# Performance work log

Hardware: AMD Instinct MI355X
Metric: run time of the kernel (lower is better)

The kernel has to match this reference:

```python
import jax, jax.numpy as jnp
import numpy as np

B, S, D, H, DFF = 4, 1024, 1024, 16, 4096
DK = D // H
EPS = 1e-5

def _ln(x, g, b):
    m = jnp.mean(x, -1, keepdims=True)
    v = jnp.mean((x - m) ** 2, -1, keepdims=True)
    return (x - m) * jax.lax.rsqrt(v + EPS) * g + b

def setup_inputs() -> dict:
    key = jax.random.key(0)
    ks = jax.random.split(key, 24)
    std = 0.02
    def w(k, shp):
        return jax.random.normal(k, shp, jnp.float32) * std
    return {
        'x': jax.random.normal(ks[0], (B, S, D), jnp.float32),
        'wq': w(ks[1], (D, D)), 'bq': jnp.zeros((D,), jnp.float32),
        'wk': w(ks[2], (D, D)), 'bk': jnp.zeros((D,), jnp.float32),
        'wv': w(ks[3], (D, D)), 'bv': jnp.zeros((D,), jnp.float32),
        'wo': w(ks[4], (D, D)), 'bo': jnp.zeros((D,), jnp.float32),
        'rel_table': jax.random.normal(ks[5], (2 * 64 - 1, H), jnp.float32),
        'g1': jnp.ones((D,), jnp.float32), 'be1': jnp.zeros((D,), jnp.float32),
        'g2': jnp.ones((D,), jnp.float32), 'be2': jnp.zeros((D,), jnp.float32),
        'w1': w(ks[6], (D, DFF)), 'b1': jnp.zeros((DFF,), jnp.float32),
        'w2': w(ks[7], (DFF, D)), 'b2': jnp.zeros((D,), jnp.float32),
        'w3': w(ks[8], (D, D)), 'b3': jnp.zeros((D,), jnp.float32),
        'gf': jnp.ones((D,), jnp.float32), 'bf': jnp.zeros((D,), jnp.float32),
    }

def reference(x, wq, bq, wk, bk, wv, bv, wo, bo, rel_table,
              g1, be1, g2, be2, w1, b1, w2, b2, w3, b3, gf, bf):
    # --- pre-norm attention ---
    nx = _ln(x, g1, be1)
    def heads(w, b):
        return (nx @ w + b).reshape(B, S, H, DK).transpose(0, 2, 1, 3)  # [B,H,S,DK]
    Q, K, V = heads(wq, bq), heads(wk, bk), heads(wv, bv)
    scores = jnp.einsum('bhsd,bhtd->bhst', Q, K) / jnp.sqrt(jnp.float32(DK))
    # relative position bias, clamped to table range
    rel = jnp.arange(S)[None, :] - jnp.arange(S)[:, None] + 63
    rel = jnp.clip(rel, 0, 2 * 64 - 2)               # [S,S]
    bias = rel_table[rel].transpose(2, 0, 1)          # [H,S,S]
    scores = scores + bias[None]
    attn = jax.nn.softmax(scores, axis=-1)
    ctx = jnp.einsum('bhst,bhtd->bhsd', attn, V)
    ctx = ctx.transpose(0, 2, 1, 3).reshape(B, S, D)
    x = x + (ctx @ wo + bo)
    # --- feed-forward (with its own inner residuals) ---
    nx2 = _ln(x, g2, be2)
    ff1 = jax.nn.gelu(nx2 @ w1 + b1, approximate=False) @ w2 + b2
    y = nx2 + ff1
    ff2 = _ln(y, gf, bf) @ w3 + b3
    ff_out = y + ff2
    return x + ff_out
```

## Files before the change

### kernel.cpp

```cpp
#include <hip/hip_runtime.h>
#include <hip/hip_bf16.h>
#include <math.h>


constexpr int Bc = 4, Sc_ = 1024, Dc = 1024, Hc = 16, DKc = 64, DFFc = 4096;
constexpr int ROWS = Bc * Sc_;
constexpr int BK = 32;

typedef short short8 __attribute__((ext_vector_type(8)));
typedef __bf16 bf16x8 __attribute__((ext_vector_type(8)));
typedef float float4v __attribute__((ext_vector_type(4)));
typedef uint uint2v __attribute__((ext_vector_type(2)));

__device__ __forceinline__ float bf2f(ushort u) {
    union { uint i; float f; } v; v.i = ((uint)u) << 16; return v.f;
}
__device__ __forceinline__ ushort f2bf(float f) {
    union { float f; uint i; } v; v.f = f;
    uint r = v.i + 0x7FFF + ((v.i >> 16) & 1);
    return (ushort)(r >> 16);
}
__device__ __forceinline__ bf16x8 as_bf(short8 s) {
    union { short8 s; bf16x8 b; } u; u.s = s; return u.b;
}
__device__ __forceinline__ uint cvt_pk_bf16(float lo, float hi) {
    uint r;
    asm("v_cvt_pk_bf16_f32 %0, %1, %2" : "=v"(r) : "v"(lo), "v"(hi));
    return r;
}
__device__ __forceinline__ float exp2_hw(float x) {
    float r;
    asm("v_exp_f32 %0, %1" : "=v"(r) : "v"(x));
    return r;
}
__device__ __forceinline__ void async_copy16(void* lds, const void* g) {
    __builtin_amdgcn_global_load_lds((const __attribute__((address_space(1))) uint*)g,
                                     (__attribute__((address_space(3))) uint*)lds, 16, 0, 0);
}
__device__ __forceinline__ float gelu_f(float v) {
    float z = v * 0.70710678118654752f;
    float az = fabsf(z);
    float t = 1.f / (1.f + 0.3275911f * az);
    float p = ((((1.061405429f * t - 1.453152027f) * t) + 1.421413741f) * t
               - 0.284496736f) * t + 0.254829592f;
    float y = 1.f - p * t * __expf(-az * az);
    float er = (z < 0.f) ? -y : y;
    return 0.5f * v * (1.f + er);
}

__global__ void sentinel_kernel(float* __restrict__ out, int n) {
    int i = blockIdx.x * 256 + threadIdx.x;
    if (i < n) out[i] = 100.0f;
}

__global__ void bias3_kernel(const float* __restrict__ a, const float* __restrict__ b,
                             const float* __restrict__ c, float* __restrict__ o) {
    int i = blockIdx.x * 256 + threadIdx.x;
    if (i < 1024) o[i] = a[i];
    else if (i < 2048) o[i] = b[i - 1024];
    else if (i < 3072) o[i] = c[i - 2048];
}

__global__ __launch_bounds__(256) void wconv_kernel(const float* __restrict__ W,
                                                    ushort* __restrict__ Wt,
                                                    int K, int N) {
    __shared__ float T[64][65];
    const int kt = blockIdx.y * 64, nt = blockIdx.x * 64;
    const int tid = threadIdx.x;
#pragma unroll
    for (int it = 0; it < 4; it++) {
        int r = it * 16 + (tid >> 4), c = (tid & 15) * 4;
        float4v v = *reinterpret_cast<const float4v*>(W + (size_t)(kt + r) * N + nt + c);
        T[r][c] = v[0]; T[r][c + 1] = v[1]; T[r][c + 2] = v[2]; T[r][c + 3] = v[3];
    }
    __syncthreads();
    int n = tid >> 2, kc = (tid & 3) * 16;
    short8 a, b;
#pragma unroll
    for (int q = 0; q < 8; q++) {
        a[q] = (short)f2bf(T[kc + q][n]);
        b[q] = (short)f2bf(T[kc + 8 + q][n]);
    }
    ushort* dst = Wt + (size_t)(nt + n) * K + kt + kc;
    *reinterpret_cast<short8*>(dst) = a;
    *reinterpret_cast<short8*>(dst + 8) = b;
}

__global__ __launch_bounds__(256) void vconv_kernel(const ushort* __restrict__ V,
                                                    ushort* __restrict__ Vt) {
    __shared__ ushort T[64][65];
    const int bh = blockIdx.y;
    const int s0 = blockIdx.x * 64;
    const int tid = threadIdx.x;
    const int r = tid >> 2, c = (tid & 3) * 16;
    const ushort* src = V + ((size_t)bh * Sc_ + s0 + r) * DKc + c;
    short8 a = *reinterpret_cast<const short8*>(src);
    short8 b = *reinterpret_cast<const short8*>(src + 8);
#pragma unroll
    for (int q = 0; q < 8; q++) { T[r][c + q] = (ushort)a[q]; T[r][c + 8 + q] = (ushort)b[q]; }
    __syncthreads();
    const int dk = tid >> 2, sc2 = (tid & 3) * 16;
    short8 o0, o1;
#pragma unroll
    for (int q = 0; q < 8; q++) { o0[q] = (short)T[sc2 + q][dk]; o1[q] = (short)T[sc2 + 8 + q][dk]; }
    ushort* dst = Vt + ((size_t)bh * DKc + dk) * Sc_ + s0 + sc2;
    *reinterpret_cast<short8*>(dst) = o0;
    *reinterpret_cast<short8*>(dst + 8) = o1;
}

template<bool IN_F32>
__global__ __launch_bounds__(256) void ln_kernel(const void* __restrict__ xin,
                                                 const float* __restrict__ g,
                                                 const float* __restrict__ be,
                                                 ushort* __restrict__ out) {
    int row = blockIdx.x;
    int tid = threadIdx.x;
    float v0[4], s = 0.f, ss = 0.f;
#pragma unroll
    for (int i = 0; i < 4; i++) {
        int c = tid + i * 256;
        float f = IN_F32 ? ((const float*)xin)[(size_t)row * Dc + c]
                         : bf2f(((const ushort*)xin)[(size_t)row * Dc + c]);
        v0[i] = f; s += f; ss += f * f;
    }
#pragma unroll
    for (int off = 32; off > 0; off >>= 1) {
        s += __shfl_down(s, off);
        ss += __shfl_down(ss, off);
    }
    __shared__ float red[8];
    __shared__ float stat[2];
    int wave = tid >> 6, lane = tid & 63;
    if (lane == 0) { red[wave] = s; red[wave + 4] = ss; }
    __syncthreads();
    if (tid == 0) {
        float a = 0.f, b = 0.f;
        for (int w = 0; w < 4; w++) { a += red[w]; b += red[w + 4]; }
        stat[0] = a; stat[1] = b;
    }
    __syncthreads();
    float mean = stat[0] * (1.f / Dc);
    float var  = stat[1] * (1.f / Dc) - mean * mean;
    float inv  = rsqrtf(var + 1e-5f);
#pragma unroll
    for (int i = 0; i < 4; i++) {
        int c = tid + i * 256;
        float nv = (v0[i] - mean) * inv * g[c] + be[c];
        out[(size_t)row * Dc + c] = f2bf(nv);
    }
}

template<int BM, int BN, typename OutT>
__global__ __launch_bounds__(256) void gemm_bt(
    const ushort* __restrict__ Ag, const ushort* __restrict__ Wt,
    const float* __restrict__ biasg,
    const float* __restrict__ res1f,
    const ushort* __restrict__ resi1, const ushort* __restrict__ resi2,
    OutT* __restrict__ outg,
    int M, int N, int K, int do_gelu, int mode) {
    constexpr int WN = BN / 64;
    constexpr int WM = 4 / WN;
    constexpr int MI = BM / (WM * 16);
    constexpr int TSZ = (BM + BN) * BK;
    constexpr int TOT = (BM + BN) * 4;
    constexpr int LPT = TOT / 256;
    constexpr unsigned VM_L = 0x0F70 | (unsigned)LPT;
    __shared__ ushort Tile[3 * TSZ];
    const int tid = threadIdx.x;
    const int wave = tid >> 6, lane = tid & 63;
    const int quad = lane >> 4, l16 = lane & 15;
    const int m0 = blockIdx.x * BM, n0 = blockIdx.y * BN;
    const int wm = (wave / WN) * (MI * 16), wn = (wave % WN) * 64;

    float4v acc[MI][4];
    const float4v zero = {0.f, 0.f, 0.f, 0.f};
#pragma unroll
    for (int i = 0; i < MI; i++)
#pragma unroll
        for (int j = 0; j < 4; j++) acc[i][j] = zero;

    auto stage = [&](int buf, int k0) {
#pragma unroll
        for (int it = 0; it < LPT; it++) {
            int c = tid + it * 256;
            int row = c >> 2, kc = (c & 3) * 8;
            const ushort* src = (row < BM)
                ? Ag + (size_t)(m0 + row) * K + k0 + kc
                : Wt + (size_t)(n0 + row - BM) * K + k0 + kc;
            async_copy16(&Tile[buf * TSZ + c * 8], src);
        }
    };

    const int nit = K / BK;
    stage(0, 0);
    stage(1, BK);
    int bc = 0, bs = 2;
    for (int i = 0; i < nit; i++) {
        __builtin_amdgcn_sched_barrier(0);
        if (i + 1 < nit) __builtin_amdgcn_s_waitcnt(VM_L);
        else             __builtin_amdgcn_s_waitcnt(0x0F70);
        __builtin_amdgcn_s_barrier();
        __builtin_amdgcn_sched_barrier(0);
        if (i + 2 < nit) stage(bs, (i + 2) * BK);
        const ushort* Asb = &Tile[bc * TSZ];
        const ushort* Bsb = &Tile[bc * TSZ + BM * BK];
        short8 af[MI], bfr[4];
#pragma unroll
        for (int ii = 0; ii < MI; ii++)
            af[ii] = *reinterpret_cast<const short8*>(&Asb[(wm + ii * 16 + l16) * BK + quad * 8]);
#pragma unroll
        for (int j = 0; j < 4; j++)
            bfr[j] = *reinterpret_cast<const short8*>(&Bsb[(wn + j * 16 + l16) * BK + quad * 8]);
#pragma unroll
        for (int j = 0; j < 4; j++)
#pragma unroll
            for (int ii = 0; ii < MI; ii++)
                acc[ii][j] = __builtin_amdgcn_mfma_f32_16x16x32_bf16(as_bf(af[ii]), as_bf(bfr[j]), acc[ii][j], 0, 0, 0);
        bc = (bc == 2) ? 0 : bc + 1;
        bs = (bs == 2) ? 0 : bs + 1;
    }
    __builtin_amdgcn_s_barrier();

#pragma unroll
    for (int j = 0; j < 4; j++) {
        int cg = n0 + wn + j * 16 + l16;
        float bv = biasg ? biasg[cg] : 0.f;
#pragma unroll
        for (int i = 0; i < MI; i++) {
#pragma unroll
            for (int r = 0; r < 4; r++) {
                int rg = m0 + wm + i * 16 + quad * 4 + r;
                float v = acc[i][j][r] + bv;
                if (do_gelu) v = gelu_f(v);
                size_t idx = (size_t)rg * N + cg;
                if (res1f) v += res1f[idx];
                if (resi1) v += bf2f(resi1[idx]);
                if (resi2) v += bf2f(resi2[idx]);
                size_t dst;
                if (mode == 1) {
                    int which = cg >> 10, wr2 = cg & 1023;
                    int h = wr2 >> 6, dk = wr2 & 63;
                    int b = rg >> 10, s = rg & 1023;
                    dst = (size_t)which * ((size_t)ROWS * Dc)
                        + (((size_t)b * Hc + h) * Sc_ + s) * DKc + dk;
                } else dst = idx;
                if constexpr (sizeof(OutT) == 4) outg[dst] = v;
                else                             outg[dst] = f2bf(v);
            }
        }
    }
}

template<typename OutT>
__global__ __launch_bounds__(512, 2) void gemm8_bt(
    const ushort* __restrict__ Ag, const ushort* __restrict__ Wt,
    const float* __restrict__ biasg, OutT* __restrict__ outg,
    int N, int K, int do_gelu, int mode) {
    __shared__ ushort Al[2][16384];
    __shared__ ushort Bl[2][16384];
    const int tid = threadIdx.x;
    const int wave = tid >> 6, lane = tid & 63;
    const int quad = lane >> 4, l16 = lane & 15;
    const int wm = (wave >> 2) * 128, wn = (wave & 3) * 64;
    const int m0 = blockIdx.y * 256, n0 = blockIdx.x * 256;

    float4v acc[8][4];
    const float4v zero = {0.f, 0.f, 0.f, 0.f};
#pragma unroll
    for (int i = 0; i < 8; i++)
#pragma unroll
        for (int j = 0; j < 4; j++) acc[i][j] = zero;

    auto stageH = [&](int buf, int k0, int which) {
#pragma unroll
        for (int it = 0; it < 2; it++) {
            int s = tid + it * 512;
            int rl = s >> 3, pch = s & 7;
            int ch = pch ^ (rl & 7);
            const ushort* src; ushort* dst;
            if (which == 0)      { int row = ((rl >> 6) << 7) + (rl & 63);
                                   src = Ag + (size_t)(m0 + row) * K + k0 + ch * 8;
                                   dst = &Al[buf][s * 8]; }
            else if (which == 1) { int row = ((rl >> 5) << 6) + (rl & 31);
                                   src = Wt + (size_t)(n0 + row) * K + k0 + ch * 8;
                                   dst = &Bl[buf][s * 8]; }
            else if (which == 2) { int row = ((rl >> 5) << 6) + 32 + (rl & 31);
                                   src = Wt + (size_t)(n0 + row) * K + k0 + ch * 8;
                                   dst = &Bl[buf][8192 + s * 8]; }
            else                 { int row = ((rl >> 6) << 7) + 64 + (rl & 63);
                                   src = Ag + (size_t)(m0 + row) * K + k0 + ch * 8;
                                   dst = &Al[buf][8192 + s * 8]; }
            async_copy16(dst, src);
        }
    };

    const int rlA = ((wm >> 7) << 6) + l16;
    const int rlB = ((wn >> 6) << 5) + l16;
    const int sw  = l16 & 7;

    const int nt = K >> 6;
    stageH(0, 0, 0); stageH(0, 0, 1); stageH(0, 0, 2); stageH(0, 0, 3);

#define G8_SYNC(WHICH, VMLAST)                                            \
    __builtin_amdgcn_sched_barrier(0);                                    \
    if (more) { stageH(nbuf, knext, WHICH);                               \
                __builtin_amdgcn_sched_barrier(0);                        \
                __builtin_amdgcn_s_waitcnt(0x0F76);         \
    } else   { __builtin_amdgcn_s_waitcnt(VMLAST); }                      \
    __builtin_amdgcn_s_barrier();                                         \
    __builtin_amdgcn_sched_barrier(0);

#define G8_COMPUTE(QM, QN, LOADA)                                         \
    if (LOADA) {                                                          \
        _Pragma("unroll") for (int kk = 0; kk < 2; kk++)                  \
        _Pragma("unroll") for (int i = 0; i < 4; i++)                     \
            af[kk][i] = *reinterpret_cast<const short8*>(                 \
                &Al[buf][(QM) * 8192 + (rlA + i * 16) * 64 +              \
                         (((kk << 2) | quad) ^ sw) * 8]);                 \
    }                                                                     \
    _Pragma("unroll") for (int kk = 0; kk < 2; kk++)                      \
    _Pragma("unroll") for (int j = 0; j < 2; j++)                         \
        bfr[kk][j] = *reinterpret_cast<const short8*>(                    \
            &Bl[buf][(QN) * 8192 + (rlB + j * 16) * 64 +                  \
                     (((kk << 2) | quad) ^ sw) * 8]);                     \
    __builtin_amdgcn_s_setprio(1);                                        \
    _Pragma("unroll") for (int kk = 0; kk < 2; kk++)                      \
    _Pragma("unroll") for (int i = 0; i < 4; i++)                         \
    _Pragma("unroll") for (int j = 0; j < 2; j++)                         \
        acc[(QM) * 4 + i][(QN) * 2 + j] =                                 \
            __builtin_amdgcn_mfma_f32_16x16x32_bf16(                      \
                as_bf(af[kk][i]), as_bf(bfr[kk][j]),                      \
                acc[(QM) * 4 + i][(QN) * 2 + j], 0, 0, 0);                \
    __builtin_amdgcn_s_setprio(0);

    for (int t = 0; t < nt; ++t) {
        const int buf = t & 1, nbuf = buf ^ 1;
        const int knext = (t + 1) << 6;
        const bool more = (t + 1 < nt);
        short8 af[2][4], bfr[2][2];
        G8_SYNC(0, 0x0F74)  G8_COMPUTE(0, 0, true)
        G8_SYNC(1, 0x0F72)  G8_COMPUTE(0, 1, false)
        G8_SYNC(2, 0x0F70)  G8_COMPUTE(1, 0, true)
        G8_SYNC(3, 0x0F70)  G8_COMPUTE(1, 1, false)
    }
#undef G8_SYNC
#undef G8_COMPUTE

#pragma unroll
    for (int jg = 0; jg < 4; jg++) {
        int cg = n0 + wn + jg * 16 + l16;
        float bv = biasg ? biasg[cg] : 0.f;
#pragma unroll
        for (int ig = 0; ig < 8; ig++) {
#pragma unroll
            for (int r = 0; r < 4; r++) {
                int rg = m0 + wm + ig * 16 + quad * 4 + r;
                float v = acc[ig][jg][r] + bv;
                if (do_gelu) v = gelu_f(v);
                size_t dst;
                if (mode == 1) {
                    int which = cg >> 10, wr2 = cg & 1023;
                    int h = wr2 >> 6, dk = wr2 & 63;
                    int b = rg >> 10, s = rg & 1023;
                    dst = (size_t)which * ((size_t)ROWS * Dc)
                        + (((size_t)b * Hc + h) * Sc_ + s) * DKc + dk;
                } else dst = (size_t)rg * N + cg;
                if constexpr (sizeof(OutT) == 4) outg[dst] = v;
                else                             outg[dst] = f2bf(v);
            }
        }
    }
}

__global__ __launch_bounds__(256, 4) void attn_kernel(
    const ushort* __restrict__ Qg, const ushort* __restrict__ Kg,
    const ushort* __restrict__ Vt, const float* __restrict__ relg,
    ushort* __restrict__ ctxg) {
    __shared__ ushort Kl[2][2048];
    __shared__ ushort Vl[2][2048];
    __shared__ float Tpad[1088];
    constexpr float L2E = 1.44269504f;

    const int blk = blockIdx.x;
    const int vb = (blk & 7) * 128 + (blk >> 3);
    const int bh = vb >> 4;
    const int qblk = vb & 15;
    const int h = bh & (Hc - 1);
    const int b = bh >> 4;
    const int qb = qblk * 64;
    const int tid = threadIdx.x;
    const int wave = tid >> 6, lane = tid & 63;
    const int quad = lane >> 4, l16 = lane & 15;
    const int ql = wave * 16 + l16;

    const ushort* Kbh  = Kg + (size_t)bh * Sc_ * DKc;
    const ushort* Vtbh = Vt + (size_t)bh * DKc * Sc_;

    auto stage = [&](int buf, int t0) {
        {
            int r = tid >> 3, ch = tid & 7;
            const ushort* src = Kbh + (size_t)(t0 + r) * DKc + ((ch ^ (r & 7)) * 8);
            async_copy16(&Kl[buf][tid * 8], src);
        }
        {
            int d = tid >> 2, ch = tid & 3;
            const ushort* src = Vtbh + (size_t)d * Sc_ + t0 + ((ch ^ ((d >> 1) & 3)) * 8);
            async_copy16(&Vl[buf][tid * 8], src);
        }
    };

    stage(0, 0);

    for (int j = tid; j < 1087; j += 256) {
        int r = min(max(j - qb, 0), 126);
        Tpad[j] = relg[r * Hc + h];
    }

    short8 aQ[2];
    {
        const ushort* qrow = Qg + ((size_t)bh * Sc_ + qb + ql) * DKc + quad * 8;
#pragma unroll
        for (int f = 0; f < 2; f++) {
            short8 v = *reinterpret_cast<const short8*>(qrow + f * 32);
#pragma unroll
            for (int e = 0; e < 8; e++) v[e] = (short)f2bf(bf2f((ushort)v[e]) * 0.125f);
            aQ[f] = v;
        }
    }
    __syncthreads();

    float4v accO[4];
#pragma unroll
    for (int i = 0; i < 4; i++) accO[i] = float4v{0.f, 0.f, 0.f, 0.f};
    float m = -1e30f, lsum = 0.f;
    float ml2 = m * L2E;
    const int srcA = ((quad & 1) * 2) * 16 + l16;
    const int srcB = srcA + 16;
    const bool hi = quad >= 2;

    auto compute = [&](int buf, int t0) {
        short8 vf[4];
#pragma unroll
        for (int dt = 0; dt < 4; dt++) {
            int d = dt * 16 + l16;
            vf[dt] = *reinterpret_cast<const short8*>(
                &Vl[buf][d * 32 + ((quad ^ ((l16 >> 1) & 3)) * 8)]);
        }
        short8 kf[2][2];
#pragma unroll
        for (int kt = 0; kt < 2; kt++)
#pragma unroll
            for (int f = 0; f < 2; f++)
                kf[kt][f] = *reinterpret_cast<const short8*>(
                    &Kl[buf][(kt * 16 + l16) * 64 + (((f * 4 + quad) ^ (l16 & 7)) * 8)]);

        const int jb = t0 + quad * 4 - ql + 63;
        float4v c0 = { Tpad[jb],      Tpad[jb + 1],  Tpad[jb + 2],  Tpad[jb + 3]  };
        float4v c1 = { Tpad[jb + 16], Tpad[jb + 17], Tpad[jb + 18], Tpad[jb + 19] };

        float4v s0 = __builtin_amdgcn_mfma_f32_16x16x32_bf16(as_bf(kf[0][0]), as_bf(aQ[0]), c0, 0, 0, 0);
        s0 = __builtin_amdgcn_mfma_f32_16x16x32_bf16(as_bf(kf[0][1]), as_bf(aQ[1]), s0, 0, 0, 0);
        float4v s1 = __builtin_amdgcn_mfma_f32_16x16x32_bf16(as_bf(kf[1][0]), as_bf(aQ[0]), c1, 0, 0, 0);
        s1 = __builtin_amdgcn_mfma_f32_16x16x32_bf16(as_bf(kf[1][1]), as_bf(aQ[1]), s1, 0, 0, 0);

        float lt = fmaxf(fmaxf(fmaxf(s0[0], s0[1]), fmaxf(s0[2], s0[3])),
                         fmaxf(fmaxf(s1[0], s1[1]), fmaxf(s1[2], s1[3])));
        if (!__all(lt <= m + 8.f)) {
            float tmax = fmaxf(lt, __shfl_xor(lt, 16));
            tmax = fmaxf(tmax, __shfl_xor(tmax, 32));
            float mn = fmaxf(m, tmax);
            float sc = exp2_hw((m - mn) * L2E);
            m = mn; ml2 = m * L2E;
            lsum *= sc;
#pragma unroll
            for (int dt = 0; dt < 4; dt++)
#pragma unroll
                for (int r = 0; r < 4; r++) accO[dt][r] *= sc;
        }
        float p0[4], p1[4];
#pragma unroll
        for (int r = 0; r < 4; r++) {
            p0[r] = exp2_hw(fmaf(s0[r], L2E, -ml2));
            p1[r] = exp2_hw(fmaf(s1[r], L2E, -ml2));
        }
        lsum += ((p0[0] + p0[1]) + (p0[2] + p0[3]))
              + ((p1[0] + p1[1]) + (p1[2] + p1[3]));

        uint w0 = cvt_pk_bf16(p0[0], p0[1]);
        uint w1 = cvt_pk_bf16(p0[2], p0[3]);
        uint w2 = cvt_pk_bf16(p1[0], p1[1]);
        uint w3 = cvt_pk_bf16(p1[2], p1[3]);
        uint a0 = __shfl(w0, srcA), a1 = __shfl(w1, srcA);
        uint a2 = __shfl(w2, srcA), a3 = __shfl(w3, srcA);
        uint b0 = __shfl(w0, srcB), b1 = __shfl(w1, srcB);
        uint b2 = __shfl(w2, srcB), b3 = __shfl(w3, srcB);
        union { uint u[4]; short8 s; } pf;
        pf.u[0] = hi ? a2 : a0;
        pf.u[1] = hi ? a3 : a1;
        pf.u[2] = hi ? b2 : b0;
        pf.u[3] = hi ? b3 : b1;

#pragma unroll
        for (int dt = 0; dt < 4; dt++)
            accO[dt] = __builtin_amdgcn_mfma_f32_16x16x32_bf16(as_bf(vf[dt]), as_bf(pf.s), accO[dt], 0, 0, 0);
    };

    for (int t0 = 0; t0 < Sc_; t0 += 64) {
        __builtin_amdgcn_sched_barrier(0);
        __builtin_amdgcn_s_waitcnt(0x0F70);
        __builtin_amdgcn_s_barrier();
        __builtin_amdgcn_sched_barrier(0);
        stage(1, t0 + 32);
        __builtin_amdgcn_sched_barrier(0);
        compute(0, t0);

        __builtin_amdgcn_sched_barrier(0);
        __builtin_amdgcn_s_waitcnt(0x0F70);
        __builtin_amdgcn_s_barrier();
        __builtin_amdgcn_sched_barrier(0);
        if (t0 + 64 < Sc_) stage(0, t0 + 64);
        __builtin_amdgcn_sched_barrier(0);
        compute(1, t0 + 32);
    }

    lsum += __shfl_xor(lsum, 16);
    lsum += __shfl_xor(lsum, 32);
    float linv = 1.f / lsum;

    const int s = qb + ql;
    ushort* orow = ctxg + ((size_t)b * Sc_ + s) * Dc + h * DKc + quad * 4;
#pragma unroll
    for (int dt = 0; dt < 4; dt++) {
        uint2v o;
        o[0] = cvt_pk_bf16(accO[dt][0] * linv, accO[dt][1] * linv);
        o[1] = cvt_pk_bf16(accO[dt][2] * linv, accO[dt][3] * linv);
        *reinterpret_cast<uint2v*>(orow + dt * 16) = o;
    }
}

extern "C" void kernel_launch(void* const* d_in, const int* in_sizes, int n_in,
                              void* d_out, int out_size, void* d_ws, size_t ws_size,
                              hipStream_t stream) {
    float* out = (float*)d_out;

    static const int exp_sizes[22] = {
        4194304, 1048576, 1024, 1048576, 1024, 1048576, 1024, 1048576, 1024,
        2032, 1024, 1024, 1024, 1024, 4194304, 4096, 4194304, 1024,
        1048576, 1024, 1024, 1024};
    bool ok = (n_in == 22);
    if (ok) for (int i = 0; i < 22; i++) if (in_sizes[i] != exp_sizes[i]) { ok = false; break; }
    if (!ok) {
        sentinel_kernel<<<(out_size + 255) / 256, 256, 0, stream>>>(out, out_size);
        return;
    }

    const float* x   = (const float*)d_in[0];
    const float* wq  = (const float*)d_in[1];  const float* bq  = (const float*)d_in[2];
    const float* wk  = (const float*)d_in[3];  const float* bk  = (const float*)d_in[4];
    const float* wv  = (const float*)d_in[5];  const float* bv  = (const float*)d_in[6];
    const float* wo  = (const float*)d_in[7];  const float* bo  = (const float*)d_in[8];
    const float* rel = (const float*)d_in[9];
    const float* g1  = (const float*)d_in[10]; const float* be1 = (const float*)d_in[11];
    const float* g2  = (const float*)d_in[12]; const float* be2 = (const float*)d_in[13];
    const float* w1  = (const float*)d_in[14]; const float* b1  = (const float*)d_in[15];
    const float* w2  = (const float*)d_in[16]; const float* b2  = (const float*)d_in[17];
    const float* w3  = (const float*)d_in[18]; const float* b3  = (const float*)d_in[19];
    const float* gf  = (const float*)d_in[20]; const float* bfp = (const float*)d_in[21];

    constexpr size_t NE = (size_t)ROWS * Dc;
    ushort* base = (ushort*)d_ws;
    ushort* Wts  = base;
    ushort* nx   = base + NE;
    ushort* Qb   = base + 2 * NE;
    ushort* Kb   = base + 3 * NE;
    ushort* Vb   = base + 4 * NE;
    ushort* Vt   = base + 5 * NE;
    float*  bqkv = (float*)(base + 6 * NE);
    ushort* ctx  = nx;
    ushort* x1   = Qb;
    ushort* nx2  = Kb;
    ushort* hb   = base + 4 * NE;
    ushort* yb   = nx;
    ushort* ly   = Kb;

    dim3 blk(256);
    dim3 blk8(512);
    dim3 gQKV(ROWS / 64, 3072 / 128);
    dim3 gD(ROWS / 64, Dc / 128);
    dim3 gFF(DFFc / 256, ROWS / 256);
    dim3 cD(Dc / 64, Dc / 64);
    dim3 c1(DFFc / 64, Dc / 64);
    dim3 c2(Dc / 64, DFFc / 64);
    dim3 cV(Sc_ / 64, Bc * Hc);

    ln_kernel<true><<<ROWS, blk, 0, stream>>>(x, g1, be1, nx);
    wconv_kernel<<<cD, blk, 0, stream>>>(wq, Wts, Dc, Dc);
    wconv_kernel<<<cD, blk, 0, stream>>>(wk, Wts + (size_t)1024 * 1024, Dc, Dc);
    wconv_kernel<<<cD, blk, 0, stream>>>(wv, Wts + (size_t)2048 * 1024, Dc, Dc);
    bias3_kernel<<<12, blk, 0, stream>>>(bq, bk, bv, bqkv);
    gemm_bt<64, 128, ushort><<<gQKV, blk, 0, stream>>>(nx, Wts, bqkv, nullptr, nullptr, nullptr, Qb, ROWS, 3072, Dc, 0, 1);
    vconv_kernel<<<cV, blk, 0, stream>>>(Vb, Vt);
    attn_kernel<<<dim3(1024), blk, 0, stream>>>(Qb, Kb, Vt, rel, ctx);
    wconv_kernel<<<cD, blk, 0, stream>>>(wo, Wts, Dc, Dc);
    gemm_bt<64, 128, ushort><<<gD, blk, 0, stream>>>(ctx, Wts, bo, x, nullptr, nullptr, x1, ROWS, Dc, Dc, 0, 0);
    ln_kernel<false><<<ROWS, blk, 0, stream>>>(x1, g2, be2, nx2);
    wconv_kernel<<<c1, blk, 0, stream>>>(w1, Wts, Dc, DFFc);
    gemm8_bt<ushort><<<gFF, blk8, 0, stream>>>(nx2, Wts, b1, hb, DFFc, Dc, 1, 0);
    wconv_kernel<<<c2, blk, 0, stream>>>(w2, Wts, DFFc, Dc);
    gemm_bt<64, 128, ushort><<<gD, blk, 0, stream>>>(hb, Wts, b2, nullptr, nx2, nullptr, yb, ROWS, Dc, DFFc, 0, 0);
    ln_kernel<false><<<ROWS, blk, 0, stream>>>(yb, gf, bfp, ly);
    wconv_kernel<<<cD, blk, 0, stream>>>(w3, Wts, Dc, Dc);
    gemm_bt<64, 128, float><<<gD, blk, 0, stream>>>(ly, Wts, b3, nullptr, x1, yb, out, ROWS, Dc, Dc, 0, 0);
}
```

Before: 442.0 us.

## Use BK=64 swizzled LDS tiles in gemm_bt and batch QKVO weight conversion

The generic GEMM gains a template K-tile depth. The D-output GEMMs now use BK=64, with an XOR swizzle on LDS chunks to avoid bank conflicts. This halves the number of barrier/wait iterations per K loop but doubles LDS per stage. The four attention weight conversions are fused into one launch, and epilogues are reordered to hoist bias loads and write rows contiguously.

```diff
diff --git a/kernel.cpp b/kernel.cpp
--- a/kernel.cpp
+++ b/kernel.cpp
@@ -5,7 +5,6 @@
 
 constexpr int Bc = 4, Sc_ = 1024, Dc = 1024, Hc = 16, DKc = 64, DFFc = 4096;
 constexpr int ROWS = Bc * Sc_;
-constexpr int BK = 32;
 
 typedef short short8 __attribute__((ext_vector_type(8)));
 typedef __bf16 bf16x8 __attribute__((ext_vector_type(8)));
@@ -82,6 +81,35 @@
         b[q] = (short)f2bf(T[kc + 8 + q][n]);
     }
     ushort* dst = Wt + (size_t)(nt + n) * K + kt + kc;
+    *reinterpret_cast<short8*>(dst) = a;
+    *reinterpret_cast<short8*>(dst + 8) = b;
+}
+
+__global__ __launch_bounds__(256) void wconv4_kernel(
+    const float* __restrict__ w0, const float* __restrict__ w1,
+    const float* __restrict__ w2, const float* __restrict__ w3,
+    ushort* __restrict__ o) {
+    __shared__ float T[64][65];
+    const int z = blockIdx.z;
+    const float* W = (z == 0) ? w0 : (z == 1) ? w1 : (z == 2) ? w2 : w3;
+    ushort* Wt = o + (size_t)z * 1024 * 1024;
+    const int kt = blockIdx.y * 64, nt = blockIdx.x * 64;
+    const int tid = threadIdx.x;
+#pragma unroll
+    for (int it = 0; it < 4; it++) {
+        int r = it * 16 + (tid >> 4), c = (tid & 15) * 4;
+        float4v v = *reinterpret_cast<const float4v*>(W + (size_t)(kt + r) * 1024 + nt + c);
+        T[r][c] = v[0]; T[r][c + 1] = v[1]; T[r][c + 2] = v[2]; T[r][c + 3] = v[3];
+    }
+    __syncthreads();
+    int n = tid >> 2, kc = (tid & 3) * 16;
+    short8 a, b;
+#pragma unroll
+    for (int q = 0; q < 8; q++) {
+        a[q] = (short)f2bf(T[kc + q][n]);
+        b[q] = (short)f2bf(T[kc + 8 + q][n]);
+    }
+    ushort* dst = Wt + (size_t)(nt + n) * 1024 + kt + kc;
     *reinterpret_cast<short8*>(dst) = a;
     *reinterpret_cast<short8*>(dst + 8) = b;
 }
@@ -150,7 +178,7 @@
     }
 }
 
-template<int BM, int BN, typename OutT>
+template<int BM, int BN, int BKt, typename OutT>
 __global__ __launch_bounds__(256) void gemm_bt(
     const ushort* __restrict__ Ag, const ushort* __restrict__ Wt,
     const float* __restrict__ biasg,
@@ -161,9 +189,11 @@
     constexpr int WN = BN / 64;
     constexpr int WM = 4 / WN;
     constexpr int MI = BM / (WM * 16);
-    constexpr int TSZ = (BM + BN) * BK;
-    constexpr int TOT = (BM + BN) * 4;
-    constexpr int LPT = TOT / 256;
+    constexpr int KS = BKt / 32;
+    constexpr int CPR = BKt / 8;
+    constexpr int TSZ = (BM + BN) * BKt;
+    constexpr int SLOTS = (BM + BN) * CPR;
+    constexpr int LPT = SLOTS / 256;
     constexpr unsigned VM_L = 0x0F70 | (unsigned)LPT;
     __shared__ ushort Tile[3 * TSZ];
     const int tid = threadIdx.x;
@@ -171,6 +201,7 @@
     const int quad = lane >> 4, l16 = lane & 15;
     const int m0 = blockIdx.x * BM, n0 = blockIdx.y * BN;
     const int wm = (wave / WN) * (MI * 16), wn = (wave % WN) * 64;
+    const int sw = l16 & 7;
 
     float4v acc[MI][4];
     const float4v zero = {0.f, 0.f, 0.f, 0.f};
@@ -182,18 +213,19 @@
     auto stage = [&](int buf, int k0) {
 #pragma unroll
         for (int it = 0; it < LPT; it++) {
-            int c = tid + it * 256;
-            int row = c >> 2, kc = (c & 3) * 8;
-            const ushort* src = (row < BM)
-                ? Ag + (size_t)(m0 + row) * K + k0 + kc
-                : Wt + (size_t)(n0 + row - BM) * K + k0 + kc;
-            async_copy16(&Tile[buf * TSZ + c * 8], src);
+            int s = tid + it * 256;
+            int r = s / CPR, pch = s % CPR;
+            int ch = (BKt == 64) ? (pch ^ (r & 7)) : pch;
+            const ushort* src = (r < BM)
+                ? Ag + (size_t)(m0 + r) * K + k0 + ch * 8
+                : Wt + (size_t)(n0 + r - BM) * K + k0 + ch * 8;
+            async_copy16(&Tile[buf * TSZ + s * 8], src);
         }
     };
 
-    const int nit = K / BK;
+    const int nit = K / BKt;
     stage(0, 0);
-    stage(1, BK);
+    stage(1, BKt);
     int bc = 0, bs = 2;
     for (int i = 0; i < nit; i++) {
         __builtin_amdgcn_sched_barrier(0);
@@ -201,36 +233,50 @@
         else             __builtin_amdgcn_s_waitcnt(0x0F70);
         __builtin_amdgcn_s_barrier();
         __builtin_amdgcn_sched_barrier(0);
-        if (i + 2 < nit) stage(bs, (i + 2) * BK);
+        if (i + 2 < nit) stage(bs, (i + 2) * BKt);
         const ushort* Asb = &Tile[bc * TSZ];
-        const ushort* Bsb = &Tile[bc * TSZ + BM * BK];
-        short8 af[MI], bfr[4];
-#pragma unroll
-        for (int ii = 0; ii < MI; ii++)
-            af[ii] = *reinterpret_cast<const short8*>(&Asb[(wm + ii * 16 + l16) * BK + quad * 8]);
-#pragma unroll
-        for (int j = 0; j < 4; j++)
-            bfr[j] = *reinterpret_cast<const short8*>(&Bsb[(wn + j * 16 + l16) * BK + quad * 8]);
-#pragma unroll
-        for (int j = 0; j < 4; j++)
-#pragma unroll
-            for (int ii = 0; ii < MI; ii++)
-                acc[ii][j] = __builtin_amdgcn_mfma_f32_16x16x32_bf16(as_bf(af[ii]), as_bf(bfr[j]), acc[ii][j], 0, 0, 0);
+        const ushort* Bsb = &Tile[bc * TSZ + BM * BKt];
+        short8 af[KS][MI], bfr[KS][4];
+#pragma unroll
+        for (int kk = 0; kk < KS; kk++) {
+#pragma unroll
+            for (int ii = 0; ii < MI; ii++) {
+                int ch = (BKt == 64) ? (((kk << 2) | quad) ^ sw) : quad;
+                af[kk][ii] = *reinterpret_cast<const short8*>(
+                    &Asb[(wm + ii * 16 + l16) * BKt + ch * 8]);
+            }
+#pragma unroll
+            for (int j = 0; j < 4; j++) {
+                int ch = (BKt == 64) ? (((kk << 2) | quad) ^ sw) : quad;
+                bfr[kk][j] = *reinterpret_cast<const short8*>(
+                    &Bsb[(wn + j * 16 + l16) * BKt + ch * 8]);
+            }
+        }
+#pragma unroll
+        for (int kk = 0; kk < KS; kk++)
+#pragma unroll
+            for (int j = 0; j < 4; j++)
+#pragma unroll
+                for (int ii = 0; ii < MI; ii++)
+                    acc[ii][j] = __builtin_amdgcn_mfma_f32_16x16x32_bf16(
+                        as_bf(af[kk][ii]), as_bf(bfr[kk][j]), acc[ii][j], 0, 0, 0);
         bc = (bc == 2) ? 0 : bc + 1;
         bs = (bs == 2) ? 0 : bs + 1;
     }
     __builtin_amdgcn_s_barrier();
 
-#pragma unroll
-    for (int j = 0; j < 4; j++) {
-        int cg = n0 + wn + j * 16 + l16;
-        float bv = biasg ? biasg[cg] : 0.f;
-#pragma unroll
-        for (int i = 0; i < MI; i++) {
-#pragma unroll
-            for (int r = 0; r < 4; r++) {
-                int rg = m0 + wm + i * 16 + quad * 4 + r;
-                float v = acc[i][j][r] + bv;
+    float bvv[4];
+#pragma unroll
+    for (int j = 0; j < 4; j++) bvv[j] = biasg ? biasg[n0 + wn + j * 16 + l16] : 0.f;
+#pragma unroll
+    for (int i = 0; i < MI; i++) {
+#pragma unroll
+        for (int r = 0; r < 4; r++) {
+            int rg = m0 + wm + i * 16 + quad * 4 + r;
+#pragma unroll
+            for (int j = 0; j < 4; j++) {
+                int cg = n0 + wn + j * 16 + l16;
+                float v = acc[i][j][r] + bvv[j];
                 if (do_gelu) v = gelu_f(v);
                 size_t idx = (size_t)rg * N + cg;
                 if (res1f) v += res1f[idx];
@@ -346,27 +392,37 @@
 #undef G8_SYNC
 #undef G8_COMPUTE
 
-#pragma unroll
-    for (int jg = 0; jg < 4; jg++) {
-        int cg = n0 + wn + jg * 16 + l16;
-        float bv = biasg ? biasg[cg] : 0.f;
-#pragma unroll
-        for (int ig = 0; ig < 8; ig++) {
-#pragma unroll
-            for (int r = 0; r < 4; r++) {
-                int rg = m0 + wm + ig * 16 + quad * 4 + r;
-                float v = acc[ig][jg][r] + bv;
-                if (do_gelu) v = gelu_f(v);
-                size_t dst;
-                if (mode == 1) {
+    float bvv[4];
+#pragma unroll
+    for (int jg = 0; jg < 4; jg++) bvv[jg] = biasg ? biasg[n0 + wn + jg * 16 + l16] : 0.f;
+#pragma unroll
+    for (int ig = 0; ig < 8; ig++) {
+#pragma unroll
+        for (int r = 0; r < 4; r++) {
+            int rg = m0 + wm + ig * 16 + quad * 4 + r;
+            if (mode == 1) {
+#pragma unroll
+                for (int jg = 0; jg < 4; jg++) {
+                    int cg = n0 + wn + jg * 16 + l16;
+                    float v = acc[ig][jg][r] + bvv[jg];
+                    if (do_gelu) v = gelu_f(v);
                     int which = cg >> 10, wr2 = cg & 1023;
                     int h = wr2 >> 6, dk = wr2 & 63;
                     int b = rg >> 10, s = rg & 1023;
-                    dst = (size_t)which * ((size_t)ROWS * Dc)
+                    size_t dst = (size_t)which * ((size_t)ROWS * Dc)
                         + (((size_t)b * Hc + h) * Sc_ + s) * DKc + dk;
-                } else dst = (size_t)rg * N + cg;
-                if constexpr (sizeof(OutT) == 4) outg[dst] = v;
-                else                             outg[dst] = f2bf(v);
+                    if constexpr (sizeof(OutT) == 4) outg[dst] = v;
+                    else                             outg[dst] = f2bf(v);
+                }
+            } else {
+                OutT* orow = outg + (size_t)rg * N + n0 + wn + l16;
+#pragma unroll
+                for (int jg = 0; jg < 4; jg++) {
+                    float v = acc[ig][jg][r] + bvv[jg];
+                    if (do_gelu) v = gelu_f(v);
+                    if constexpr (sizeof(OutT) == 4) orow[jg * 16] = v;
+                    else                             orow[jg * 16] = f2bf(v);
+                }
             }
         }
     }
@@ -588,27 +644,25 @@
     dim3 gQKV(ROWS / 64, 3072 / 128);
     dim3 gD(ROWS / 64, Dc / 128);
     dim3 gFF(DFFc / 256, ROWS / 256);
-    dim3 cD(Dc / 64, Dc / 64);
+    dim3 c4(16, 16, 4);
     dim3 c1(DFFc / 64, Dc / 64);
     dim3 c2(Dc / 64, DFFc / 64);
+    dim3 cD(Dc / 64, Dc / 64);
     dim3 cV(Sc_ / 64, Bc * Hc);
 
+    wconv4_kernel<<<c4, blk, 0, stream>>>(wq, wk, wv, wo, Wts);
+    bias3_kernel<<<12, blk, 0, stream>>>(bq, bk, bv, bqkv);
     ln_kernel<true><<<ROWS, blk, 0, stream>>>(x, g1, be1, nx);
-    wconv_kernel<<<cD, blk, 0, stream>>>(wq, Wts, Dc, Dc);
-    wconv_kernel<<<cD, blk, 0, stream>>>(wk, Wts + (size_t)1024 * 1024, Dc, Dc);
-    wconv_kernel<<<cD, blk, 0, stream>>>(wv, Wts + (size_t)2048 * 1024, Dc, Dc);
-    bias3_kernel<<<12, blk, 0, stream>>>(bq, bk, bv, bqkv);
-    gemm_bt<64, 128, ushort><<<gQKV, blk, 0, stream>>>(nx, Wts, bqkv, nullptr, nullptr, nullptr, Qb, ROWS, 3072, Dc, 0, 1);
+    gemm_bt<64, 128, 32, ushort><<<gQKV, blk, 0, stream>>>(nx, Wts, bqkv, nullptr, nullptr, nullptr, Qb, ROWS, 3072, Dc, 0, 1);
     vconv_kernel<<<cV, blk, 0, stream>>>(Vb, Vt);
     attn_kernel<<<dim3(1024), blk, 0, stream>>>(Qb, Kb, Vt, rel, ctx);
-    wconv_kernel<<<cD, blk, 0, stream>>>(wo, Wts, Dc, Dc);
-    gemm_bt<64, 128, ushort><<<gD, blk, 0, stream>>>(ctx, Wts, bo, x, nullptr, nullptr, x1, ROWS, Dc, Dc, 0, 0);
+    gemm_bt<64, 128, 64, ushort><<<gD, blk, 0, stream>>>(ctx, Wts + (size_t)3 * 1024 * 1024, bo, x, nullptr, nullptr, x1, ROWS, Dc, Dc, 0, 0);
     ln_kernel<false><<<ROWS, blk, 0, stream>>>(x1, g2, be2, nx2);
     wconv_kernel<<<c1, blk, 0, stream>>>(w1, Wts, Dc, DFFc);
     gemm8_bt<ushort><<<gFF, blk8, 0, stream>>>(nx2, Wts, b1, hb, DFFc, Dc, 1, 0);
     wconv_kernel<<<c2, blk, 0, stream>>>(w2, Wts, DFFc, Dc);
-    gemm_bt<64, 128, ushort><<<gD, blk, 0, stream>>>(hb, Wts, b2, nullptr, nx2, nullptr, yb, ROWS, Dc, DFFc, 0, 0);
+    gemm_bt<64, 128, 64, ushort><<<gD, blk, 0, stream>>>(hb, Wts, b2, nullptr, nx2, nullptr, yb, ROWS, Dc, DFFc, 0, 0);
     ln_kernel<false><<<ROWS, blk, 0, stream>>>(yb, gf, bfp, ly);
     wconv_kernel<<<cD, blk, 0, stream>>>(w3, Wts, Dc, Dc);
-    gemm_bt<64, 128, float><<<gD, blk, 0, stream>>>(ly, Wts, b3, nullptr, x1, yb, out, ROWS, Dc, Dc, 0, 0);
-}
+    gemm_bt<64, 128, 64, float><<<gD, blk, 0, stream>>>(ly, Wts, b3, nullptr, x1, yb, out, ROWS, Dc, Dc, 0, 0);
+}
```

Result: faster. 406.8 us (-8.0%).
